# Kernel optimization log

Hardware: AMD Instinct MI355X
Metric: run time of the kernel (lower is better)

## Reference

```python
import jax, jax.numpy as jnp
import numpy as np

T, B, D, H = 128, 32, 1024, 1024


def setup_inputs() -> dict:
    key = jax.random.key(0)
    k1, k2, k3 = jax.random.split(key, 3)
    s_in = 1.0 / np.sqrt(D)
    s_h = 1.0 / np.sqrt(H)
    x = jax.random.normal(k1, (T, B, D), dtype=jnp.float32)
    Wx = jax.random.normal(k2, (D, 4 * H), dtype=jnp.float32) * s_in
    Wh = jax.random.normal(k3, (H, 4 * H), dtype=jnp.float32) * s_h
    b = jnp.zeros((4 * H,), dtype=jnp.float32)
    return {"x": x, "Wx": Wx, "Wh": Wh, "b": b}


def reference(x, Wx, Wh, b):
    # RNN.forward with alpha=1 (scheduled-sampling branch dead) and future=0:
    # pure unroll of the LSTM cell over time dim 0, hidden starts at zero
    # (prev_hidden=None after reset()). hard=False -> sigmoid/tanh.
    Bsz = x.shape[1]
    h0 = jnp.zeros((Bsz, H), dtype=x.dtype)
    c0 = jnp.zeros((Bsz, H), dtype=x.dtype)

    def step(carry, xt):
        h, c = carry
        gates = xt @ Wx + h @ Wh + b  # [B, 4H]
        i, f, g, o = jnp.split(gates, 4, axis=-1)
        c_new = jax.nn.sigmoid(f) * c + jax.nn.sigmoid(i) * jnp.tanh(g)
        h_new = jax.nn.sigmoid(o) * jnp.tanh(c_new)
        return (h_new, c_new), h_new

    _, hs = jax.lax.scan(step, (h0, c0), x)  # hs: [T, B, H]
    return hs
```

## Files before the change

kernel.cpp:

```cpp
#include <hip/hip_runtime.h>
#include <hip/hip_bf16.h>
#include <stdint.h>

#define T_STEPS 128
#define BATCH   32
#define DIM     1024
#define HID     1024
#define NGATE   4096
#define MROWS   4096
#define NWGR    64

typedef unsigned int u32;
typedef __attribute__((ext_vector_type(8)))  __bf16 bf16x8;
typedef __attribute__((ext_vector_type(4)))  float  f32x4;
typedef __attribute__((ext_vector_type(16))) float  f32x16;
typedef __attribute__((ext_vector_type(4)))  u32    u32x4;

__device__ __forceinline__ unsigned short f2bf(float f) {
    u32 x = __float_as_uint(f);
    return (unsigned short)((x + 0x7fffu + ((x >> 16) & 1u)) >> 16);
}
__device__ __forceinline__ float sigf(float x) {
    return 1.0f / (1.0f + __expf(-x));
}
__device__ __forceinline__ float tanh_fast(float x) {
    float ax = fabsf(x);
    float e  = __expf(-2.0f * ax);
    float t  = (1.0f - e) / (1.0f + e);
    return copysignf(t, x);
}
__device__ __forceinline__ u32 umax2(u32 a, u32 b) { return a > b ? a : b; }

__device__ __forceinline__ void store_u32_coh(u32* p, u32 v) {
    asm volatile("global_store_dword %0, %1, off sc1" :: "v"(p), "v"(v) : "memory");
}


__global__ void cast_f32_bf16(const float* __restrict__ in,
                              unsigned short* __restrict__ out, int n) {
    int idx = (blockIdx.x * blockDim.x + threadIdx.x) * 4;
    if (idx + 3 < n) {
        float4 v = *(const float4*)(in + idx);
        ushort4 o;
        o.x = f2bf(v.x); o.y = f2bf(v.y); o.z = f2bf(v.z); o.w = f2bf(v.w);
        *(ushort4*)(out + idx) = o;
    }
}

__global__ void fill_sentinel(u32* __restrict__ p, int n) {
    int i = (blockIdx.x * blockDim.x + threadIdx.x) * 4;
    if (i + 3 < n) {
        u32x4 v = {0xFFFFFFFFu, 0xFFFFFFFFu, 0xFFFFFFFFu, 0xFFFFFFFFu};
        *(u32x4*)(p + i) = v;
    }
}

__global__ void transpose_cast(const float* __restrict__ in,
                               unsigned short* __restrict__ out, int R, int C) {
    __shared__ float tile[32][33];
    int c0 = blockIdx.x * 32, r0 = blockIdx.y * 32;
    int tx = threadIdx.x, ty = threadIdx.y;
#pragma unroll
    for (int i = 0; i < 4; ++i)
        tile[ty + i * 8][tx] = in[(size_t)(r0 + ty + i * 8) * C + c0 + tx];
    __syncthreads();
#pragma unroll
    for (int i = 0; i < 4; ++i)
        out[(size_t)(c0 + ty + i * 8) * R + r0 + tx] = f2bf(tile[tx][ty + i * 8]);
}

__global__ __launch_bounds__(256) void gemm_xw(
    const unsigned short* __restrict__ A,
    const unsigned short* __restrict__ BT,
    const float* __restrict__ bias,
    float* __restrict__ Gp) {
    __shared__ unsigned short As[128 * 32];
    __shared__ unsigned short Bs[128 * 32];
    int tid  = threadIdx.x;
    int wave = tid >> 6, lane = tid & 63;
    int q = lane >> 4, c = lane & 15;
    int wm = wave >> 1, wn = wave & 1;
    int tm = blockIdx.y * 128, tn = blockIdx.x * 128;

    f32x4 acc[4][4] = {};

    const int srow0 = tid >> 2;
    const int srow1 = 64 + (tid >> 2);
    const int scol  = (tid & 3) * 8;

    u32x4 ra0, ra1, rb0, rb1;
    ra0 = *(const u32x4*)(A  + (size_t)(tm + srow0) * DIM + scol);
    ra1 = *(const u32x4*)(A  + (size_t)(tm + srow1) * DIM + scol);
    rb0 = *(const u32x4*)(BT + (size_t)(tn + srow0) * DIM + scol);
    rb1 = *(const u32x4*)(BT + (size_t)(tn + srow1) * DIM + scol);

    for (int kk = 0; kk < 32; ++kk) {
        __syncthreads();
        *(u32x4*)(As + srow0 * 32 + scol) = ra0;
        *(u32x4*)(As + srow1 * 32 + scol) = ra1;
        *(u32x4*)(Bs + srow0 * 32 + scol) = rb0;
        *(u32x4*)(Bs + srow1 * 32 + scol) = rb1;
        __syncthreads();
        if (kk < 31) {
            int ko = (kk + 1) * 32 + scol;
            ra0 = *(const u32x4*)(A  + (size_t)(tm + srow0) * DIM + ko);
            ra1 = *(const u32x4*)(A  + (size_t)(tm + srow1) * DIM + ko);
            rb0 = *(const u32x4*)(BT + (size_t)(tn + srow0) * DIM + ko);
            rb1 = *(const u32x4*)(BT + (size_t)(tn + srow1) * DIM + ko);
        }
        bf16x8 af[4], bfv[4];
#pragma unroll
        for (int i = 0; i < 4; ++i) {
            af[i]  = *(const bf16x8*)(As + (wm * 64 + i * 16 + c) * 32 + q * 8);
            bfv[i] = *(const bf16x8*)(Bs + (wn * 64 + i * 16 + c) * 32 + q * 8);
        }
#pragma unroll
        for (int i = 0; i < 4; ++i)
#pragma unroll
            for (int j = 0; j < 4; ++j)
                acc[i][j] = __builtin_amdgcn_mfma_f32_16x16x32_bf16(
                    af[i], bfv[j], acc[i][j], 0, 0, 0);
    }
#pragma unroll
    for (int j = 0; j < 4; ++j) {
        int co = tn + wn * 64 + j * 16 + c;
        float bj = bias[co];
        int g = co >> 10, hu = co & 1023;
        int wgr = hu >> 4, u = hu & 15;
        int cp = u * 4 + g;
#pragma unroll
        for (int i = 0; i < 4; ++i) {
            int row0 = tm + wm * 64 + i * 16 + q * 4;
#pragma unroll
            for (int r = 0; r < 4; ++r)
                Gp[((size_t)wgr * MROWS + row0 + r) * 64 + cp] = acc[i][j][r] + bj;
        }
    }
}

__global__ __launch_bounds__(512, 1) void lstm_rec(
    const unsigned short* __restrict__ WhT,
    const float* __restrict__ Gp,
    unsigned short* hb,
    float* __restrict__ out) {
    __shared__ unsigned short Hs[32][1024];
    __shared__ float SlT[8][32][64];
    __shared__ unsigned short Ht[32][16];
    const int wg = blockIdx.x, tid = threadIdx.x;
    const int wv = tid >> 6, lane = tid & 63;
    const int ln = lane & 31, lh = lane >> 5;

    bf16x8 br0[8], br1[8];
    {
        const int u8 = ln >> 2, g = ln & 3;
        const unsigned short* w0 =
            WhT + (size_t)(g * HID + wg * 16 + 0 * 8 + u8) * DIM + wv * 128 + lh * 8;
        const unsigned short* w1 =
            WhT + (size_t)(g * HID + wg * 16 + 1 * 8 + u8) * DIM + wv * 128 + lh * 8;
#pragma unroll
        for (int kk = 0; kk < 8; ++kk) {
            br0[kk] = *(const bf16x8*)(w0 + kk * 16);
            br1[kk] = *(const bf16x8*)(w1 + kk * 16);
        }
    }

    const int batch = tid >> 4, uu = tid & 15;
    float cs = 0.f;
    f32x4 ga = *(const f32x4*)(Gp + ((size_t)wg * MROWS + batch) * 64 + uu * 4);

    char* hs_base = (char*)&Hs[0][0];
    const int rxor = (ln & 15) << 4;

    for (int t = 0; t < T_STEPS; ++t) {
        if (t > 0) {
            const char* p0 = (const char*)hb + ((size_t)t << 16)
                           + ((size_t)wv << 13) + (size_t)lane * 16;
            const char* p1 = p0 + 4096;
            u32x4 h[8];
            for (;;) {
                asm volatile(
                    "global_load_dwordx4 %0, %8, off sc1\n\t"
                    "global_load_dwordx4 %1, %8, off offset:1024 sc1\n\t"
                    "global_load_dwordx4 %2, %8, off offset:2048 sc1\n\t"
                    "global_load_dwordx4 %3, %8, off offset:3072 sc1\n\t"
                    "global_load_dwordx4 %4, %9, off sc1\n\t"
                    "global_load_dwordx4 %5, %9, off offset:1024 sc1\n\t"
                    "global_load_dwordx4 %6, %9, off offset:2048 sc1\n\t"
                    "global_load_dwordx4 %7, %9, off offset:3072 sc1\n\t"
                    "s_waitcnt vmcnt(0)"
                    : "=&v"(h[0]), "=&v"(h[1]), "=&v"(h[2]), "=&v"(h[3]),
                      "=&v"(h[4]), "=&v"(h[5]), "=&v"(h[6]), "=&v"(h[7])
                    : "v"(p0), "v"(p1)
                    : "memory");
                u32 m = 0;
#pragma unroll
                for (int i = 0; i < 8; ++i) {
                    u32 a = umax2(umax2(h[i][0], h[i][1]),
                                  umax2(h[i][2], h[i][3]));
                    m = umax2(m, a);
                }
                if (!__any((int)(m == 0xFFFFFFFFu))) break;
            }
#pragma unroll
            for (int j = 0; j < 8; ++j) {
                int row  = (wv << 2) + (j >> 1);
                int colb = ((j & 1) << 10) + lane * 16;
                int off  = (row << 11) + (colb ^ ((row & 15) << 4));
                *(u32x4*)(hs_base + off) = h[j];
            }
            asm volatile("s_waitcnt lgkmcnt(0)" ::: "memory");
            __builtin_amdgcn_s_barrier();

            f32x16 acc0 = {}, acc1 = {};
            const char* hrow = hs_base + (ln << 11);
#pragma unroll
            for (int kk = 0; kk < 8; ++kk) {
                int cb = ((wv << 8) + (kk << 5) + (lh << 4)) ^ rxor;
                bf16x8 a = *(const bf16x8*)(hrow + cb);
                acc0 = __builtin_amdgcn_mfma_f32_32x32x16_bf16(a, br0[kk], acc0, 0, 0, 0);
                acc1 = __builtin_amdgcn_mfma_f32_32x32x16_bf16(a, br1[kk], acc1, 0, 0, 0);
            }

#pragma unroll
            for (int rg = 0; rg < 4; ++rg)
#pragma unroll
                for (int rr = 0; rr < 4; ++rr) {
                    const int bb = rg * 8 + lh * 4 + rr;
                    SlT[wv][bb][ln]      = acc0[rg * 4 + rr];
                    SlT[wv][bb][32 + ln] = acc1[rg * 4 + rr];
                }
            asm volatile("s_waitcnt lgkmcnt(0)" ::: "memory");
            __builtin_amdgcn_s_barrier();
        }

        f32x4 gv = ga;
        if (t > 0) {
#pragma unroll
            for (int ks = 0; ks < 8; ++ks)
                gv += *(const f32x4*)&SlT[ks][batch][uu * 4];
        }
        float cn = sigf(gv[1]) * cs + sigf(gv[0]) * tanh_fast(gv[2]);
        cs = cn;
        float hv = sigf(gv[3]) * tanh_fast(cn);

        Ht[batch][uu] = f2bf(hv);
        asm volatile("s_waitcnt lgkmcnt(0)" ::: "memory");
        if ((uu & 1) == 0) {
            u32 packed = *(const u32*)&Ht[batch][uu];
            store_u32_coh((u32*)(hb + (size_t)(t + 1) * (BATCH * HID)
                                    + (size_t)batch * HID + wg * 16 + uu), packed);
        }

        if (t + 1 < T_STEPS)
            ga = *(const f32x4*)(Gp + ((size_t)wg * MROWS + (size_t)(t + 1) * 32 + batch) * 64
                                 + uu * 4);
        out[((size_t)t * BATCH + batch) * HID + wg * 16 + uu] = hv;
    }
}


extern "C" void kernel_launch(void* const* d_in, const int* in_sizes, int n_in,
                              void* d_out, int out_size, void* d_ws, size_t ws_size,
                              hipStream_t stream) {
    const float* x  = (const float*)d_in[0];
    const float* Wx = (const float*)d_in[1];
    const float* Wh = (const float*)d_in[2];
    const float* b  = (const float*)d_in[3];
    float* out = (float*)d_out;

    char* ws = (char*)d_ws;
    const size_t OFF_XBF  = 0;
    const size_t OFF_WXT  = 8ull  << 20;
    const size_t OFF_WHT  = 16ull << 20;
    const size_t OFF_G    = 24ull << 20;
    const size_t OFF_HB   = 88ull << 20;
    const size_t NEEDED   = OFF_HB + (size_t)(T_STEPS + 1) * BATCH * HID * 2;
    if (ws_size < NEEDED) return;

    unsigned short* xbf = (unsigned short*)(ws + OFF_XBF);
    unsigned short* WxT = (unsigned short*)(ws + OFF_WXT);
    unsigned short* WhT = (unsigned short*)(ws + OFF_WHT);
    float*          Gp  = (float*)(ws + OFF_G);
    unsigned short* hb  = (unsigned short*)(ws + OFF_HB);

    cast_f32_bf16<<<(MROWS * DIM / 4 + 255) / 256, 256, 0, stream>>>(x, xbf, MROWS * DIM);
    const int HBW = (T_STEPS + 1) * BATCH * HID / 2;
    fill_sentinel<<<(HBW / 4 + 255) / 256, 256, 0, stream>>>((u32*)hb, HBW);
    dim3 tb(32, 8);
    transpose_cast<<<dim3(NGATE / 32, DIM / 32), tb, 0, stream>>>(Wx, WxT, DIM, NGATE);
    transpose_cast<<<dim3(NGATE / 32, HID / 32), tb, 0, stream>>>(Wh, WhT, HID, NGATE);

    gemm_xw<<<dim3(NGATE / 128, MROWS / 128), 256, 0, stream>>>(xbf, WxT, b, Gp);

    lstm_rec<<<NWGR, 512, 0, stream>>>(WhT, Gp, hb, out);
}
```

Measured before the change: 495.7 us.

## Split recurrent step into two batch halves to pipeline poll, MFMA and gate math

Each timestep is split into two 16-row batch halves. Each half polls its own part of the previous hidden state, runs the MFMA over it and computes its gates, so the second half's wait and compute overlap the first half's publish. Output stores and the next Gp prefetch are moved into the spin-wait window of the other half. LDS staging through Ht is replaced by a lane shuffle to pack the bf16 pairs. The cost is twice the barriers and MFMA passes per step, each still producing full 32-row accumulators of which only half are used, plus more complex indexing.

Result: slower. 630.7 us (+27.2%).

```diff
diff --git a/kernel.cpp b/kernel.cpp
--- a/kernel.cpp
+++ b/kernel.cpp
@@ -144,11 +144,11 @@
     unsigned short* hb,
     float* __restrict__ out) {
     __shared__ unsigned short Hs[32][1024];
-    __shared__ float SlT[8][32][64];
-    __shared__ unsigned short Ht[32][16];
+    __shared__ float SlT[8][16][64];
     const int wg = blockIdx.x, tid = threadIdx.x;
     const int wv = tid >> 6, lane = tid & 63;
     const int ln = lane & 31, lh = lane >> 5;
+    const int myhalf = wv >> 2;
 
     bf16x8 br0[8], br1[8];
     {
@@ -166,96 +166,108 @@
 
     const int batch = tid >> 4, uu = tid & 15;
     float cs = 0.f;
+    float hvp = 0.f;
     f32x4 ga = *(const f32x4*)(Gp + ((size_t)wg * MROWS + batch) * 64 + uu * 4);
 
     char* hs_base = (char*)&Hs[0][0];
     const int rxor = (ln & 15) << 4;
 
     for (int t = 0; t < T_STEPS; ++t) {
-        if (t > 0) {
-            const char* p0 = (const char*)hb + ((size_t)t << 16)
-                           + ((size_t)wv << 13) + (size_t)lane * 16;
-            const char* p1 = p0 + 4096;
-            u32x4 h[8];
-            for (;;) {
-                asm volatile(
-                    "global_load_dwordx4 %0, %8, off sc1\n\t"
-                    "global_load_dwordx4 %1, %8, off offset:1024 sc1\n\t"
-                    "global_load_dwordx4 %2, %8, off offset:2048 sc1\n\t"
-                    "global_load_dwordx4 %3, %8, off offset:3072 sc1\n\t"
-                    "global_load_dwordx4 %4, %9, off sc1\n\t"
-                    "global_load_dwordx4 %5, %9, off offset:1024 sc1\n\t"
-                    "global_load_dwordx4 %6, %9, off offset:2048 sc1\n\t"
-                    "global_load_dwordx4 %7, %9, off offset:3072 sc1\n\t"
-                    "s_waitcnt vmcnt(0)"
-                    : "=&v"(h[0]), "=&v"(h[1]), "=&v"(h[2]), "=&v"(h[3]),
-                      "=&v"(h[4]), "=&v"(h[5]), "=&v"(h[6]), "=&v"(h[7])
-                    : "v"(p0), "v"(p1)
-                    : "memory");
-                u32 m = 0;
-#pragma unroll
-                for (int i = 0; i < 8; ++i) {
-                    u32 a = umax2(umax2(h[i][0], h[i][1]),
-                                  umax2(h[i][2], h[i][3]));
-                    m = umax2(m, a);
-                }
-                if (!__any((int)(m == 0xFFFFFFFFu))) break;
+#pragma unroll
+        for (int X = 0; X < 2; ++X) {
+            f32x16 acc0 = {}, acc1 = {};
+            if (t > 0) {
+                const char* p0 = (const char*)hb + ((size_t)t << 16) + (X << 15)
+                               + (wv << 12) + (size_t)lane * 16;
+                u32x4 h[4];
+                for (;;) {
+                    asm volatile(
+                        "global_load_dwordx4 %0, %4, off sc1\n\t"
+                        "global_load_dwordx4 %1, %4, off offset:1024 sc1\n\t"
+                        "global_load_dwordx4 %2, %4, off offset:2048 sc1\n\t"
+                        "global_load_dwordx4 %3, %4, off offset:3072 sc1\n\t"
+                        "s_waitcnt vmcnt(0)"
+                        : "=&v"(h[0]), "=&v"(h[1]), "=&v"(h[2]), "=&v"(h[3])
+                        : "v"(p0)
+                        : "memory");
+                    u32 m = 0;
+#pragma unroll
+                    for (int i = 0; i < 4; ++i) {
+                        u32 a = umax2(umax2(h[i][0], h[i][1]),
+                                      umax2(h[i][2], h[i][3]));
+                        m = umax2(m, a);
+                    }
+                    if (!__any((int)(m == 0xFFFFFFFFu))) break;
+                }
+
+                if (myhalf != X) {
+                    const int to = X ? t : (t - 1);
+                    out[((size_t)to * BATCH + batch) * HID + wg * 16 + uu] = hvp;
+                    const int tg = X ? ((t + 1 < T_STEPS) ? t + 1 : T_STEPS - 1) : t;
+                    ga = *(const f32x4*)(Gp + ((size_t)wg * MROWS
+                            + (size_t)tg * 32 + batch) * 64 + uu * 4);
+                }
+
+#pragma unroll
+                for (int j = 0; j < 4; ++j) {
+                    int row  = X * 16 + (wv << 1) + (j >> 1);
+                    int colb = ((j & 1) << 10) + lane * 16;
+                    int off  = (row << 11) + (colb ^ ((row & 15) << 4));
+                    *(u32x4*)(hs_base + off) = h[j];
+                }
+                asm volatile("s_waitcnt lgkmcnt(0)" ::: "memory");
+                __builtin_amdgcn_s_barrier();
+
+                const char* hrow = hs_base + (ln << 11);
+#pragma unroll
+                for (int kk = 0; kk < 8; ++kk) {
+                    int cb = ((wv << 8) + (kk << 5) + (lh << 4)) ^ rxor;
+                    bf16x8 a = *(const bf16x8*)(hrow + cb);
+                    acc0 = __builtin_amdgcn_mfma_f32_32x32x16_bf16(a, br0[kk], acc0, 0, 0, 0);
+                    acc1 = __builtin_amdgcn_mfma_f32_32x32x16_bf16(a, br1[kk], acc1, 0, 0, 0);
+                }
+
+#pragma unroll
+                for (int rg2 = 0; rg2 < 2; ++rg2)
+#pragma unroll
+                    for (int rr = 0; rr < 4; ++rr) {
+                        const int bl = rr + 8 * rg2 + 4 * lh;
+                        SlT[wv][bl][ln]      = acc0[(2 * X + rg2) * 4 + rr];
+                        SlT[wv][bl][32 + ln] = acc1[(2 * X + rg2) * 4 + rr];
+                    }
+                asm volatile("s_waitcnt lgkmcnt(0)" ::: "memory");
+                __builtin_amdgcn_s_barrier();
+            } else if (X == 1) {
+                if (myhalf == 0) {
+                    out[(size_t)batch * HID + wg * 16 + uu] = hvp;
+                    ga = *(const f32x4*)(Gp + ((size_t)wg * MROWS + 32 + batch) * 64
+                                         + uu * 4);
+                }
             }
-#pragma unroll
-            for (int j = 0; j < 8; ++j) {
-                int row  = (wv << 2) + (j >> 1);
-                int colb = ((j & 1) << 10) + lane * 16;
-                int off  = (row << 11) + (colb ^ ((row & 15) << 4));
-                *(u32x4*)(hs_base + off) = h[j];
+
+            if (myhalf == X) {
+                f32x4 gv = ga;
+                if (t > 0) {
+#pragma unroll
+                    for (int ks = 0; ks < 8; ++ks)
+                        gv += *(const f32x4*)&SlT[ks][batch & 15][uu * 4];
+                }
+                float cn = sigf(gv[1]) * cs + sigf(gv[0]) * tanh_fast(gv[2]);
+                cs = cn;
+                float hv = sigf(gv[3]) * tanh_fast(cn);
+                u32 hw = (u32)f2bf(hv);
+                u32 pw = (u32)__shfl_xor((int)hw, 1, 64);
+                if ((lane & 1) == 0) {
+                    store_u32_coh((u32*)(hb + (size_t)(t + 1) * (BATCH * HID)
+                                            + (size_t)batch * HID + wg * 16 + uu),
+                                  hw | (pw << 16));
+                }
+                hvp = hv;
             }
-            asm volatile("s_waitcnt lgkmcnt(0)" ::: "memory");
-            __builtin_amdgcn_s_barrier();
-
-            f32x16 acc0 = {}, acc1 = {};
-            const char* hrow = hs_base + (ln << 11);
-#pragma unroll
-            for (int kk = 0; kk < 8; ++kk) {
-                int cb = ((wv << 8) + (kk << 5) + (lh << 4)) ^ rxor;
-                bf16x8 a = *(const bf16x8*)(hrow + cb);
-                acc0 = __builtin_amdgcn_mfma_f32_32x32x16_bf16(a, br0[kk], acc0, 0, 0, 0);
-                acc1 = __builtin_amdgcn_mfma_f32_32x32x16_bf16(a, br1[kk], acc1, 0, 0, 0);
-            }
-
-#pragma unroll
-            for (int rg = 0; rg < 4; ++rg)
-#pragma unroll
-                for (int rr = 0; rr < 4; ++rr) {
-                    const int bb = rg * 8 + lh * 4 + rr;
-                    SlT[wv][bb][ln]      = acc0[rg * 4 + rr];
-                    SlT[wv][bb][32 + ln] = acc1[rg * 4 + rr];
-                }
-            asm volatile("s_waitcnt lgkmcnt(0)" ::: "memory");
-            __builtin_amdgcn_s_barrier();
-        }
-
-        f32x4 gv = ga;
-        if (t > 0) {
-#pragma unroll
-            for (int ks = 0; ks < 8; ++ks)
-                gv += *(const f32x4*)&SlT[ks][batch][uu * 4];
-        }
-        float cn = sigf(gv[1]) * cs + sigf(gv[0]) * tanh_fast(gv[2]);
-        cs = cn;
-        float hv = sigf(gv[3]) * tanh_fast(cn);
-
-        Ht[batch][uu] = f2bf(hv);
-        asm volatile("s_waitcnt lgkmcnt(0)" ::: "memory");
-        if ((uu & 1) == 0) {
-            u32 packed = *(const u32*)&Ht[batch][uu];
-            store_u32_coh((u32*)(hb + (size_t)(t + 1) * (BATCH * HID)
-                                    + (size_t)batch * HID + wg * 16 + uu), packed);
-        }
-
-        if (t + 1 < T_STEPS)
-            ga = *(const f32x4*)(Gp + ((size_t)wg * MROWS + (size_t)(t + 1) * 32 + batch) * 64
-                                 + uu * 4);
-        out[((size_t)t * BATCH + batch) * HID + wg * 16 + uu] = hv;
-    }
+        }
+    }
+    if (myhalf == 1)
+        out[((size_t)(T_STEPS - 1) * BATCH + batch) * HID + wg * 16 + uu] = hvp;
 }
 
 
```

## Fuse x bf16 cast into input GEMM and interleave gate rows in transpose

Applied to the files above, without the earlier changes.

Removes the separate cast_f32_bf16 kernel by having gemm_xw load fp32 x directly and convert to bf16 while staging into shared memory. The weight transposes now write gate-interleaved row order (unit*4+gate), so the GEMM epilogue and the recurrent kernel's weight loads use simple contiguous indexing. This saves a kernel launch and an extra pass over x, but doubles the global load bytes for the A operand inside the GEMM and adds conversion ALU work there.

New measurement: 480.1 us. 1.03x faster.

```diff
diff --git a/kernel.cpp b/kernel.cpp
--- a/kernel.cpp
+++ b/kernel.cpp
@@ -36,17 +36,6 @@
 }
 
 
-__global__ void cast_f32_bf16(const float* __restrict__ in,
-                              unsigned short* __restrict__ out, int n) {
-    int idx = (blockIdx.x * blockDim.x + threadIdx.x) * 4;
-    if (idx + 3 < n) {
-        float4 v = *(const float4*)(in + idx);
-        ushort4 o;
-        o.x = f2bf(v.x); o.y = f2bf(v.y); o.z = f2bf(v.z); o.w = f2bf(v.w);
-        *(ushort4*)(out + idx) = o;
-    }
-}
-
 __global__ void fill_sentinel(u32* __restrict__ p, int n) {
     int i = (blockIdx.x * blockDim.x + threadIdx.x) * 4;
     if (i + 3 < n) {
@@ -65,12 +54,15 @@
         tile[ty + i * 8][tx] = in[(size_t)(r0 + ty + i * 8) * C + c0 + tx];
     __syncthreads();
 #pragma unroll
-    for (int i = 0; i < 4; ++i)
-        out[(size_t)(c0 + ty + i * 8) * R + r0 + tx] = f2bf(tile[tx][ty + i * 8]);
+    for (int i = 0; i < 4; ++i) {
+        int cc = c0 + ty + i * 8;
+        int rp = ((cc & 1023) << 2) | (cc >> 10);
+        out[(size_t)rp * R + r0 + tx] = f2bf(tile[tx][ty + i * 8]);
+    }
 }
 
 __global__ __launch_bounds__(256) void gemm_xw(
-    const unsigned short* __restrict__ A,
+    const float* __restrict__ A,
     const unsigned short* __restrict__ BT,
     const float* __restrict__ bias,
     float* __restrict__ Gp) {
@@ -88,23 +80,38 @@
     const int srow1 = 64 + (tid >> 2);
     const int scol  = (tid & 3) * 8;
 
-    u32x4 ra0, ra1, rb0, rb1;
-    ra0 = *(const u32x4*)(A  + (size_t)(tm + srow0) * DIM + scol);
-    ra1 = *(const u32x4*)(A  + (size_t)(tm + srow1) * DIM + scol);
+    float4 a0l, a0h, a1l, a1h;
+    u32x4 rb0, rb1;
+    a0l = *(const float4*)(A + (size_t)(tm + srow0) * DIM + scol);
+    a0h = *(const float4*)(A + (size_t)(tm + srow0) * DIM + scol + 4);
+    a1l = *(const float4*)(A + (size_t)(tm + srow1) * DIM + scol);
+    a1h = *(const float4*)(A + (size_t)(tm + srow1) * DIM + scol + 4);
     rb0 = *(const u32x4*)(BT + (size_t)(tn + srow0) * DIM + scol);
     rb1 = *(const u32x4*)(BT + (size_t)(tn + srow1) * DIM + scol);
 
     for (int kk = 0; kk < 32; ++kk) {
         __syncthreads();
-        *(u32x4*)(As + srow0 * 32 + scol) = ra0;
-        *(u32x4*)(As + srow1 * 32 + scol) = ra1;
-        *(u32x4*)(Bs + srow0 * 32 + scol) = rb0;
-        *(u32x4*)(Bs + srow1 * 32 + scol) = rb1;
+        {
+            u32x4 pa0 = { (u32)f2bf(a0l.x) | ((u32)f2bf(a0l.y) << 16),
+                          (u32)f2bf(a0l.z) | ((u32)f2bf(a0l.w) << 16),
+                          (u32)f2bf(a0h.x) | ((u32)f2bf(a0h.y) << 16),
+                          (u32)f2bf(a0h.z) | ((u32)f2bf(a0h.w) << 16) };
+            u32x4 pa1 = { (u32)f2bf(a1l.x) | ((u32)f2bf(a1l.y) << 16),
+                          (u32)f2bf(a1l.z) | ((u32)f2bf(a1l.w) << 16),
+                          (u32)f2bf(a1h.x) | ((u32)f2bf(a1h.y) << 16),
+                          (u32)f2bf(a1h.z) | ((u32)f2bf(a1h.w) << 16) };
+            *(u32x4*)(As + srow0 * 32 + scol) = pa0;
+            *(u32x4*)(As + srow1 * 32 + scol) = pa1;
+            *(u32x4*)(Bs + srow0 * 32 + scol) = rb0;
+            *(u32x4*)(Bs + srow1 * 32 + scol) = rb1;
+        }
         __syncthreads();
         if (kk < 31) {
             int ko = (kk + 1) * 32 + scol;
-            ra0 = *(const u32x4*)(A  + (size_t)(tm + srow0) * DIM + ko);
-            ra1 = *(const u32x4*)(A  + (size_t)(tm + srow1) * DIM + ko);
+            a0l = *(const float4*)(A + (size_t)(tm + srow0) * DIM + ko);
+            a0h = *(const float4*)(A + (size_t)(tm + srow0) * DIM + ko + 4);
+            a1l = *(const float4*)(A + (size_t)(tm + srow1) * DIM + ko);
+            a1h = *(const float4*)(A + (size_t)(tm + srow1) * DIM + ko + 4);
             rb0 = *(const u32x4*)(BT + (size_t)(tn + srow0) * DIM + ko);
             rb1 = *(const u32x4*)(BT + (size_t)(tn + srow1) * DIM + ko);
         }
@@ -124,10 +131,8 @@
 #pragma unroll
     for (int j = 0; j < 4; ++j) {
         int co = tn + wn * 64 + j * 16 + c;
-        float bj = bias[co];
-        int g = co >> 10, hu = co & 1023;
-        int wgr = hu >> 4, u = hu & 15;
-        int cp = u * 4 + g;
+        float bj = bias[(co & 3) * 1024 + (co >> 2)];
+        int wgr = co >> 6, cp = co & 63;
 #pragma unroll
         for (int i = 0; i < 4; ++i) {
             int row0 = tm + wm * 64 + i * 16 + q * 4;
@@ -152,11 +157,10 @@
 
     bf16x8 br0[8], br1[8];
     {
-        const int u8 = ln >> 2, g = ln & 3;
         const unsigned short* w0 =
-            WhT + (size_t)(g * HID + wg * 16 + 0 * 8 + u8) * DIM + wv * 128 + lh * 8;
+            WhT + (size_t)(wg * 64 + ln) * DIM + wv * 128 + lh * 8;
         const unsigned short* w1 =
-            WhT + (size_t)(g * HID + wg * 16 + 1 * 8 + u8) * DIM + wv * 128 + lh * 8;
+            WhT + (size_t)(wg * 64 + 32 + ln) * DIM + wv * 128 + lh * 8;
 #pragma unroll
         for (int kk = 0; kk < 8; ++kk) {
             br0[kk] = *(const bf16x8*)(w0 + kk * 16);
@@ -269,7 +273,6 @@
     float* out = (float*)d_out;
 
     char* ws = (char*)d_ws;
-    const size_t OFF_XBF  = 0;
     const size_t OFF_WXT  = 8ull  << 20;
     const size_t OFF_WHT  = 16ull << 20;
     const size_t OFF_G    = 24ull << 20;
@@ -277,20 +280,18 @@
     const size_t NEEDED   = OFF_HB + (size_t)(T_STEPS + 1) * BATCH * HID * 2;
     if (ws_size < NEEDED) return;
 
-    unsigned short* xbf = (unsigned short*)(ws + OFF_XBF);
     unsigned short* WxT = (unsigned short*)(ws + OFF_WXT);
     unsigned short* WhT = (unsigned short*)(ws + OFF_WHT);
     float*          Gp  = (float*)(ws + OFF_G);
     unsigned short* hb  = (unsigned short*)(ws + OFF_HB);
 
-    cast_f32_bf16<<<(MROWS * DIM / 4 + 255) / 256, 256, 0, stream>>>(x, xbf, MROWS * DIM);
     const int HBW = (T_STEPS + 1) * BATCH * HID / 2;
     fill_sentinel<<<(HBW / 4 + 255) / 256, 256, 0, stream>>>((u32*)hb, HBW);
     dim3 tb(32, 8);
     transpose_cast<<<dim3(NGATE / 32, DIM / 32), tb, 0, stream>>>(Wx, WxT, DIM, NGATE);
     transpose_cast<<<dim3(NGATE / 32, HID / 32), tb, 0, stream>>>(Wh, WhT, HID, NGATE);
 
-    gemm_xw<<<dim3(NGATE / 128, MROWS / 128), 256, 0, stream>>>(xbf, WxT, b, Gp);
+    gemm_xw<<<dim3(NGATE / 128, MROWS / 128), 256, 0, stream>>>(x, WxT, b, Gp);
 
     lstm_rec<<<NWGR, 512, 0, stream>>>(WhT, Gp, hb, out);
 }
```

## Use direct global-to-LDS loads in input GEMM and interleave gate rows in transposed weights

Applied to the files above, without the earlier changes.

The input-projection GEMM now loads A and B tiles with global_load_lds (16-byte direct-to-LDS) instead of staging them through registers with software prefetch. The transpose-cast kernel permutes weight rows so the four gates of each hidden unit sit next to each other. That simplifies the GEMM epilogue scatter and the recurrent kernel's weight indexing. The aim is to cut register pressure and VGPR-to-LDS copy instructions in the GEMM. The cost is losing the overlap of the next tile's global load with current MFMA work, since loads now sit between barriers.

Measured after the change: 468.7 us. 5.4% less time.

```diff
diff --git a/kernel.cpp b/kernel.cpp
--- a/kernel.cpp
+++ b/kernel.cpp
@@ -33,6 +33,12 @@
 
 __device__ __forceinline__ void store_u32_coh(u32* p, u32 v) {
     asm volatile("global_store_dword %0, %1, off sc1" :: "v"(p), "v"(v) : "memory");
+}
+
+__device__ __forceinline__ void gload16(void* lds, const void* g) {
+    __builtin_amdgcn_global_load_lds(
+        (const __attribute__((address_space(1))) unsigned int*)g,
+        (__attribute__((address_space(3))) unsigned int*)lds, 16, 0, 0);
 }
 
 
@@ -65,8 +71,11 @@
         tile[ty + i * 8][tx] = in[(size_t)(r0 + ty + i * 8) * C + c0 + tx];
     __syncthreads();
 #pragma unroll
-    for (int i = 0; i < 4; ++i)
-        out[(size_t)(c0 + ty + i * 8) * R + r0 + tx] = f2bf(tile[tx][ty + i * 8]);
+    for (int i = 0; i < 4; ++i) {
+        int cc = c0 + ty + i * 8;
+        int rp = ((cc & 1023) << 2) | (cc >> 10);
+        out[(size_t)rp * R + r0 + tx] = f2bf(tile[tx][ty + i * 8]);
+    }
 }
 
 __global__ __launch_bounds__(256) void gemm_xw(
@@ -76,38 +85,33 @@
     float* __restrict__ Gp) {
     __shared__ unsigned short As[128 * 32];
     __shared__ unsigned short Bs[128 * 32];
-    int tid  = threadIdx.x;
-    int wave = tid >> 6, lane = tid & 63;
-    int q = lane >> 4, c = lane & 15;
-    int wm = wave >> 1, wn = wave & 1;
-    int tm = blockIdx.y * 128, tn = blockIdx.x * 128;
+    const int tid = threadIdx.x;
+    const int wv = tid >> 6, lane = tid & 63;
+    const int q = lane >> 4, c = lane & 15;
+    const int wm = wv >> 1, wn = wv & 1;
+    const int tm = blockIdx.y * 128, tn = blockIdx.x * 128;
 
     f32x4 acc[4][4] = {};
 
-    const int srow0 = tid >> 2;
-    const int srow1 = 64 + (tid >> 2);
-    const int scol  = (tid & 3) * 8;
-
-    u32x4 ra0, ra1, rb0, rb1;
-    ra0 = *(const u32x4*)(A  + (size_t)(tm + srow0) * DIM + scol);
-    ra1 = *(const u32x4*)(A  + (size_t)(tm + srow1) * DIM + scol);
-    rb0 = *(const u32x4*)(BT + (size_t)(tn + srow0) * DIM + scol);
-    rb1 = *(const u32x4*)(BT + (size_t)(tn + srow1) * DIM + scol);
+    const int rA = (wv * 2) * 16 + (lane >> 2);
+    const int cb = (lane & 3) * 16;
+    const char* gA0 = (const char*)A  + (size_t)(tm + rA) * (DIM * 2) + cb;
+    const char* gA1 = gA0 + (size_t)16 * DIM * 2;
+    const char* gB0 = (const char*)BT + (size_t)(tn + rA) * (DIM * 2) + cb;
+    const char* gB1 = gB0 + (size_t)16 * DIM * 2;
+    char* lA0 = (char*)As + (wv * 2 + 0) * 1024;
+    char* lA1 = (char*)As + (wv * 2 + 1) * 1024;
+    char* lB0 = (char*)Bs + (wv * 2 + 0) * 1024;
+    char* lB1 = (char*)Bs + (wv * 2 + 1) * 1024;
 
     for (int kk = 0; kk < 32; ++kk) {
+        const size_t ko = (size_t)kk * 64;
         __syncthreads();
-        *(u32x4*)(As + srow0 * 32 + scol) = ra0;
-        *(u32x4*)(As + srow1 * 32 + scol) = ra1;
-        *(u32x4*)(Bs + srow0 * 32 + scol) = rb0;
-        *(u32x4*)(Bs + srow1 * 32 + scol) = rb1;
+        gload16(lA0, gA0 + ko);
+        gload16(lA1, gA1 + ko);
+        gload16(lB0, gB0 + ko);
+        gload16(lB1, gB1 + ko);
         __syncthreads();
-        if (kk < 31) {
-            int ko = (kk + 1) * 32 + scol;
-            ra0 = *(const u32x4*)(A  + (size_t)(tm + srow0) * DIM + ko);
-            ra1 = *(const u32x4*)(A  + (size_t)(tm + srow1) * DIM + ko);
-            rb0 = *(const u32x4*)(BT + (size_t)(tn + srow0) * DIM + ko);
-            rb1 = *(const u32x4*)(BT + (size_t)(tn + srow1) * DIM + ko);
-        }
         bf16x8 af[4], bfv[4];
 #pragma unroll
         for (int i = 0; i < 4; ++i) {
@@ -124,10 +128,8 @@
 #pragma unroll
     for (int j = 0; j < 4; ++j) {
         int co = tn + wn * 64 + j * 16 + c;
-        float bj = bias[co];
-        int g = co >> 10, hu = co & 1023;
-        int wgr = hu >> 4, u = hu & 15;
-        int cp = u * 4 + g;
+        float bj = bias[(co & 3) * 1024 + (co >> 2)];
+        int wgr = co >> 6, cp = co & 63;
 #pragma unroll
         for (int i = 0; i < 4; ++i) {
             int row0 = tm + wm * 64 + i * 16 + q * 4;
@@ -152,11 +154,10 @@
 
     bf16x8 br0[8], br1[8];
     {
-        const int u8 = ln >> 2, g = ln & 3;
         const unsigned short* w0 =
-            WhT + (size_t)(g * HID + wg * 16 + 0 * 8 + u8) * DIM + wv * 128 + lh * 8;
+            WhT + (size_t)(wg * 64 + ln) * DIM + wv * 128 + lh * 8;
         const unsigned short* w1 =
-            WhT + (size_t)(g * HID + wg * 16 + 1 * 8 + u8) * DIM + wv * 128 + lh * 8;
+            WhT + (size_t)(wg * 64 + 32 + ln) * DIM + wv * 128 + lh * 8;
 #pragma unroll
         for (int kk = 0; kk < 8; ++kk) {
             br0[kk] = *(const bf16x8*)(w0 + kk * 16);
```
